# Kernel tuning notes

Measured on AMD Instinct MI355X. Metric: run time of the kernel, lower is better.

Reference implementation:

```python
import jax, jax.numpy as jnp
import numpy as np

N, E, H_DIM, HEADS = 20000, 640000, 128, 8
HD = H_DIM // HEADS  # head_dim = 16


def setup_inputs() -> dict:
    key = jax.random.key(0)
    ks = jax.random.split(key, 12)
    def xavier(k, shape):
        fan_in, fan_out = shape[0], shape[1]
        lim = jnp.sqrt(6.0 / (fan_in + fan_out))
        return jax.random.uniform(k, shape, jnp.float32, -lim, lim)
    return {
        "x": jax.random.normal(ks[0], (N, H_DIM), jnp.float32),
        "edge_index": jax.random.randint(ks[1], (2, E), 0, N, jnp.int64 if jax.config.x64_enabled else jnp.int32),
        "edge_attr": jax.random.normal(ks[2], (E, H_DIM), jnp.float32),
        "WQ": xavier(ks[3], (H_DIM, H_DIM)),
        "WK": xavier(ks[4], (H_DIM, H_DIM)),
        "WV": xavier(ks[5], (H_DIM, H_DIM)),
        "WE": xavier(ks[6], (H_DIM, H_DIM)),
        "Wout": xavier(ks[7], (H_DIM, H_DIM)),
        "bout": jnp.zeros((H_DIM,), jnp.float32),
        "gn_w": jnp.ones((H_DIM,), jnp.float32),
        "gn_b": jnp.zeros((H_DIM,), jnp.float32),
        "gn_ms": jnp.ones((H_DIM,), jnp.float32),
    }


def reference(x, edge_index, edge_attr, WQ, WK, WV, WE, Wout, bout, gn_w, gn_b, gn_ms):
    n = x.shape[0]
    src, dst = edge_index[0], edge_index[1]  # PyG: row=source j, col=target i

    q = (x @ WQ).reshape(n, HEADS, HD)
    k = (x @ WK).reshape(n, HEADS, HD)
    v = (x @ WV).reshape(n, HEADS, HD)
    e = (edge_attr @ WE).reshape(-1, HEADS, HD)

    # per-edge attention score [E, HEADS]
    score = jnp.sum(q[dst] * (k[src] + e), axis=-1) / jnp.sqrt(jnp.asarray(HD, x.dtype))

    # scatter-softmax over edges grouped by destination node
    seg_max = jax.ops.segment_max(score, dst, num_segments=n)  # [N, HEADS]
    seg_max = jnp.where(jnp.isfinite(seg_max), seg_max, 0.0)
    ex = jnp.exp(score - seg_max[dst])
    denom = jax.ops.segment_sum(ex, dst, num_segments=n)
    alpha = ex / (denom[dst] + 1e-16)  # [E, HEADS]

    # weighted scatter-add aggregation
    msg = alpha[..., None] * (v[src] + e)  # [E, HEADS, HD]
    out = jax.ops.segment_sum(msg, dst, num_segments=n).reshape(n, H_DIM)

    out = out @ Wout + bout
    h = out + x  # residual (DropPath is identity in eval)

    # GraphNorm with batch=None -> single-graph normalization
    mean = jnp.mean(h, axis=0)
    o = h - mean * gn_ms
    var = jnp.mean(o * o, axis=0)
    o = gn_w * o / jnp.sqrt(var + 1e-5) + gn_b

    return jax.nn.gelu(o, approximate=False)
```

## Files before the change

kernel.cpp:

```cpp
#include <hip/hip_runtime.h>

using u16 = unsigned short;
using u32 = unsigned int;
typedef float f32x4 __attribute__((ext_vector_type(4)));
typedef float f32x2 __attribute__((ext_vector_type(2)));
typedef short s16x8 __attribute__((ext_vector_type(8)));
typedef u32   u32x2 __attribute__((ext_vector_type(2)));
typedef u32   u32x4 __attribute__((ext_vector_type(4)));

__device__ __forceinline__ u16 f2bf(float f) {
  u32 u = __float_as_uint(f);
  u += 0x7fffu + ((u >> 16) & 1u);
  return (u16)(u >> 16);
}
__device__ __forceinline__ float bf2f(u16 h) {
  return __uint_as_float(((u32)h) << 16);
}

__global__ void ROEN_Final_33526514713351_kernel() {}


__global__ void roen_prep_w(const float* __restrict__ W0, const float* __restrict__ W1,
                            const float* __restrict__ W2, const float* __restrict__ W3,
                            const float* __restrict__ W4, u16* __restrict__ Wt,
                            int* __restrict__ count, int N, float* __restrict__ dbg) {
  int b = blockIdx.x;
  if (b < 5) {
    if (b == 0 && threadIdx.x == 0) dbg[4] = 1004.0f;
    const float* W = (b == 0) ? W0 : (b == 1) ? W1 : (b == 2) ? W2 : (b == 3) ? W3 : W4;
    for (int idx = threadIdx.x; idx < 16384; idx += 256) {
      int n = idx >> 7, k = idx & 127;
      Wt[b * 16384 + idx] = f2bf(W[k * 128 + n]);
    }
  } else {
    int i = (b - 5) * 256 + threadIdx.x;
    if (i == 0) dbg[0] = 1000.0f;
    if (i < N) count[i] = 0;
  }
}

__global__ void roen_hist(const int* __restrict__ ei, int E, int* __restrict__ count,
                          int* __restrict__ rank, float* __restrict__ dbg) {
  int i = blockIdx.x * 256 + threadIdx.x;
  if (i == 0) dbg[1] = 1001.0f;
  if (i < E) rank[i] = atomicAdd(&count[ei[E + i]], 1);
}

__global__ __launch_bounds__(1024) void roen_scan(const int* __restrict__ count, int N,
                                                  int* __restrict__ off,
                                                  float* __restrict__ dbg) {
  __shared__ int wsum[16];
  __shared__ int carrys;
  int tid = threadIdx.x, lane = tid & 63, wv = tid >> 6;
  if (tid == 0) { dbg[2] = 1002.0f; carrys = 0; }
  __syncthreads();
  for (int base = 0; base < N; base += 1024) {
    int i = base + tid;
    int v = (i < N) ? count[i] : 0;
    int x = v;
#pragma unroll
    for (int s = 1; s < 64; s <<= 1) {
      int t = __shfl_up(x, s);
      if (lane >= s) x += t;
    }
    if (lane == 63) wsum[wv] = x;
    __syncthreads();
    if (wv == 0 && lane < 16) {
      int y = wsum[lane];
#pragma unroll
      for (int s = 1; s < 16; s <<= 1) {
        int t = __shfl_up(y, s);
        if (lane >= s) y += t;
      }
      wsum[lane] = y;
    }
    __syncthreads();
    int wbase = (wv == 0) ? 0 : wsum[wv - 1];
    int incl = x + wbase + carrys;
    if (i < N) off[i] = incl - v;
    __syncthreads();
    if (tid == 1023) carrys = incl;
    __syncthreads();
  }
  if (tid == 0) off[N] = carrys;
}

__global__ void roen_scatter(const int* __restrict__ ei, const int* __restrict__ off,
                             const int* __restrict__ rank, int E,
                             int* __restrict__ inv, int* __restrict__ srcS,
                             int* __restrict__ dstS, float* __restrict__ dbg) {
  int i = blockIdx.x * 256 + threadIdx.x;
  if (i == 0) dbg[3] = 1003.0f;
  if (i < E) {
    int d = ei[E + i];
    int p = off[d] + rank[i];
    inv[i] = p;
    srcS[p] = ei[i];
    dstS[p] = d;
  }
}

__global__ __launch_bounds__(256) void roen_gemm_qkv(const float* __restrict__ x,
                                                     const u16* __restrict__ Wt,
                                                     u16* __restrict__ qb, u16* __restrict__ kb,
                                                     u32* __restrict__ vb2, int M,
                                                     float* __restrict__ dbg) {
  __shared__ u16 As[64 * 128];
  const int tid = threadIdx.x;
  if (blockIdx.x == 0 && tid == 0) dbg[5] = 1005.0f;
  const long brow = (long)blockIdx.x * 64;

  {
    f32x4 tmp[8];
#pragma unroll
    for (int j = 0; j < 8; ++j) {
      int idx = j * 256 + tid;
      int row = idx >> 5;
      int c4 = (idx & 31) * 4;
      long grow = brow + row;
      f32x4 a = {0.f, 0.f, 0.f, 0.f};
      if (grow < M) a = *(const f32x4*)(x + grow * 128 + c4);
      tmp[j] = a;
    }
#pragma unroll
    for (int j = 0; j < 8; ++j) {
      int idx = j * 256 + tid;
      int row = idx >> 5;
      int c4 = (idx & 31) * 4;
      u32 lo = ((u32)f2bf(tmp[j][1]) << 16) | (u32)f2bf(tmp[j][0]);
      u32 hi = ((u32)f2bf(tmp[j][3]) << 16) | (u32)f2bf(tmp[j][2]);
      int byte = (row * 256 + c4 * 2) ^ ((row & 7) << 4);
      u32x2 val; val[0] = lo; val[1] = hi;
      *(u32x2*)((char*)As + byte) = val;
    }
  }
  __syncthreads();

  const int wave = tid >> 6, lane = tid & 63;
  const int wc = wave * 32;
  const int lr = lane & 15, lg = lane >> 4;

  s16x8 af[4][4];
#pragma unroll
  for (int ks = 0; ks < 4; ++ks) {
    int kb2 = (ks * 32 + lg * 8) * 2;
#pragma unroll
    for (int mt = 0; mt < 4; ++mt) {
      int row = mt * 16 + lr;
      int byte = (row * 256 + kb2) ^ ((row & 7) << 4);
      af[ks][mt] = *(const s16x8*)((const char*)As + byte);
    }
  }

  for (int w = 0; w < 3; ++w) {
    s16x8 bfr[4][2];
#pragma unroll
    for (int ks = 0; ks < 4; ++ks)
#pragma unroll
      for (int nt = 0; nt < 2; ++nt)
        bfr[ks][nt] = *(const s16x8*)(Wt + w * 16384 + (wc + nt * 16 + lr) * 128 + ks * 32 + lg * 8);

    f32x4 acc[4][2];
    for (int mt = 0; mt < 4; ++mt)
      for (int nt = 0; nt < 2; ++nt) acc[mt][nt] = {0.f, 0.f, 0.f, 0.f};

#pragma unroll
    for (int ks = 0; ks < 4; ++ks)
      for (int mt = 0; mt < 4; ++mt)
        for (int nt = 0; nt < 2; ++nt)
          acc[mt][nt] = __builtin_amdgcn_mfma_f32_16x16x32_bf16(af[ks][mt], bfr[ks][nt], acc[mt][nt], 0, 0, 0);

    if (w == 2) {
      for (int mt = 0; mt < 4; ++mt) {
        for (int r = 0; r < 4; ++r) {
          long row = brow + mt * 16 + lg * 4 + r;
          if (row < M) {
            u32 val = (u32)f2bf(acc[mt][0][r]) | ((u32)f2bf(acc[mt][1][r]) << 16);
            vb2[row * 64 + wave * 16 + lr] = val;
          }
        }
      }
    } else {
      u16* C = (w == 0) ? qb : kb;
      for (int mt = 0; mt < 4; ++mt) {
        for (int nt = 0; nt < 2; ++nt) {
          int col = wc + nt * 16 + lr;
          for (int r = 0; r < 4; ++r) {
            long row = brow + mt * 16 + lg * 4 + r;
            if (row < M) C[row * 128 + col] = f2bf(acc[mt][nt][r]);
          }
        }
      }
    }
  }
}

__global__ __launch_bounds__(256) void roen_gemm_e(const float* __restrict__ ea,
                                                   const u16* __restrict__ WtE,
                                                   const int* __restrict__ inv,
                                                   u32* __restrict__ eS2, int E,
                                                   float* __restrict__ dbg) {
  __shared__ u16 As[64 * 128];
  __shared__ int invv[64];
  const int tid = threadIdx.x;
  if (blockIdx.x == 0 && tid == 0) dbg[6] = 1006.0f;
  const long brow = (long)blockIdx.x * 64;

  if (tid < 64) {
    long pos = brow + tid;
    invv[tid] = (pos < E) ? inv[pos] : -1;
  }

  {
    f32x4 tmp[8];
#pragma unroll
    for (int j = 0; j < 8; ++j) {
      int idx = j * 256 + tid;
      int row = idx >> 5;
      int c4 = (idx & 31) * 4;
      long grow = brow + row;
      f32x4 a = {0.f, 0.f, 0.f, 0.f};
      if (grow < E) a = *(const f32x4*)(ea + grow * 128 + c4);
      tmp[j] = a;
    }
#pragma unroll
    for (int j = 0; j < 8; ++j) {
      int idx = j * 256 + tid;
      int row = idx >> 5;
      int c4 = (idx & 31) * 4;
      u32 lo = ((u32)f2bf(tmp[j][1]) << 16) | (u32)f2bf(tmp[j][0]);
      u32 hi = ((u32)f2bf(tmp[j][3]) << 16) | (u32)f2bf(tmp[j][2]);
      int byte = (row * 256 + c4 * 2) ^ ((row & 7) << 4);
      u32x2 val; val[0] = lo; val[1] = hi;
      *(u32x2*)((char*)As + byte) = val;
    }
  }
  __syncthreads();

  const int wave = tid >> 6, lane = tid & 63;
  const int wc = wave * 32;
  const int lr = lane & 15, lg = lane >> 4;

  s16x8 bfr[4][2];
#pragma unroll
  for (int ks = 0; ks < 4; ++ks)
#pragma unroll
    for (int nt = 0; nt < 2; ++nt)
      bfr[ks][nt] = *(const s16x8*)(WtE + (wc + nt * 16 + lr) * 128 + ks * 32 + lg * 8);

  f32x4 acc[4][2];
  for (int mt = 0; mt < 4; ++mt)
    for (int nt = 0; nt < 2; ++nt) acc[mt][nt] = {0.f, 0.f, 0.f, 0.f};

  for (int ks = 0; ks < 4; ++ks) {
    int kb2 = (ks * 32 + lg * 8) * 2;
    s16x8 af[4];
    for (int mt = 0; mt < 4; ++mt) {
      int row = mt * 16 + lr;
      int byte = (row * 256 + kb2) ^ ((row & 7) << 4);
      af[mt] = *(const s16x8*)((const char*)As + byte);
    }
    for (int mt = 0; mt < 4; ++mt)
      for (int nt = 0; nt < 2; ++nt)
        acc[mt][nt] = __builtin_amdgcn_mfma_f32_16x16x32_bf16(af[mt], bfr[ks][nt], acc[mt][nt], 0, 0, 0);
  }

  for (int mt = 0; mt < 4; ++mt) {
    for (int r = 0; r < 4; ++r) {
      int row = mt * 16 + lg * 4 + r;
      int op = invv[row];
      if (op >= 0) {
        u32 val = (u32)f2bf(acc[mt][0][r]) | ((u32)f2bf(acc[mt][1][r]) << 16);
        eS2[(long)op * 64 + wave * 16 + lr] = val;
      }
    }
  }
}

__global__ __launch_bounds__(256) void roen_score(const int* __restrict__ srcS,
                                                  const int* __restrict__ dstS,
                                                  const u16* __restrict__ qb,
                                                  const u16* __restrict__ kb,
                                                  const u32* __restrict__ eS2,
                                                  float* __restrict__ wS, int E,
                                                  float* __restrict__ dbg) {
  long gid = (long)blockIdx.x * 256 + threadIdx.x;
  if (gid == 0) dbg[9] = 1009.0f;
  long pos = gid >> 3;
  int h = (int)(gid & 7);
  if (pos >= E) return;
  int dst = dstS[pos], src = srcS[pos];
  const s16x8* qp = (const s16x8*)(qb + (long)dst * 128 + h * 16);
  const s16x8* kp = (const s16x8*)(kb + (long)src * 128 + h * 16);
  const u32x4* ep = (const u32x4*)(eS2 + (long)pos * 64 + (h >> 1) * 16);
  const int sh = (h & 1) * 16;
  float acc = 0.f;
#pragma unroll
  for (int c = 0; c < 2; ++c) {
    s16x8 qv = qp[c], kv = kp[c];
    u32x4 ea_ = ep[c * 2], eb_ = ep[c * 2 + 1];
#pragma unroll
    for (int j = 0; j < 4; ++j) {
      float e0 = bf2f((u16)(ea_[j] >> sh));
      float e1 = bf2f((u16)(eb_[j] >> sh));
      acc += bf2f((u16)qv[j]) * (bf2f((u16)kv[j]) + e0);
      acc += bf2f((u16)qv[j + 4]) * (bf2f((u16)kv[j + 4]) + e1);
    }
  }
  wS[pos * 8 + h] = __expf(fminf(acc * 0.25f, 80.f));
}

__global__ __launch_bounds__(256) void roen_node_agg(const int* __restrict__ off,
                                                     const int* __restrict__ srcS,
                                                     const u32* __restrict__ eS2,
                                                     const u32* __restrict__ vb2,
                                                     const float* __restrict__ wS,
                                                     u16* __restrict__ outat, int N,
                                                     float* __restrict__ dbg) {
  int wave = threadIdx.x >> 6;
  int lane = threadIdx.x & 63;
  int node = blockIdx.x * 4 + wave;
  if (node == 0 && lane == 0) dbg[10] = 1010.0f;
  if (node >= N) return;
  int beg = off[node], end = off[node + 1];

  const int dA = 32 * (lane >> 4) + (lane & 15);
  const int dB = dA + 16;
  const int hA = dA >> 4;
  float accA = 0.f, accB = 0.f, dsA = 0.f, dsB = 0.f;

  int pos = beg;
  for (; pos + 8 <= end; pos += 8) {
    int ss[8];
    f32x2 w[8];
    u32 ev[8], vv[8];
#pragma unroll
    for (int i = 0; i < 8; ++i) ss[i] = srcS[pos + i];
#pragma unroll
    for (int i = 0; i < 8; ++i) w[i] = *(const f32x2*)(wS + (long)(pos + i) * 8 + hA);
#pragma unroll
    for (int i = 0; i < 8; ++i) ev[i] = eS2[(long)(pos + i) * 64 + lane];
#pragma unroll
    for (int i = 0; i < 8; ++i) vv[i] = vb2[(long)ss[i] * 64 + lane];
#pragma unroll
    for (int i = 0; i < 8; ++i) {
      accA += w[i][0] * (bf2f((u16)vv[i]) + bf2f((u16)ev[i]));
      accB += w[i][1] * (bf2f((u16)(vv[i] >> 16)) + bf2f((u16)(ev[i] >> 16)));
      dsA += w[i][0]; dsB += w[i][1];
    }
  }
  for (; pos < end; ++pos) {
    f32x2 w = *(const f32x2*)(wS + (long)pos * 8 + hA);
    u32 ev = eS2[(long)pos * 64 + lane];
    int src = srcS[pos];
    u32 vv = vb2[(long)src * 64 + lane];
    accA += w[0] * (bf2f((u16)vv) + bf2f((u16)ev));
    accB += w[1] * (bf2f((u16)(vv >> 16)) + bf2f((u16)(ev >> 16)));
    dsA += w[0]; dsB += w[1];
  }
  outat[(long)node * 128 + dA] = f2bf(accA / (dsA + 1e-16f));
  outat[(long)node * 128 + dB] = f2bf(accB / (dsB + 1e-16f));
}

__global__ __launch_bounds__(256) void roen_gemm_out(const u16* __restrict__ A,
                                                     const u16* __restrict__ Wt,
                                                     const float* __restrict__ x,
                                                     const float* __restrict__ bo,
                                                     float* __restrict__ h,
                                                     float* __restrict__ psum,
                                                     float* __restrict__ psumsq, int M,
                                                     float* __restrict__ dbg) {
  __shared__ u16 As[64 * 128];
  const int tid = threadIdx.x;
  if (blockIdx.x == 0 && tid == 0) dbg[11] = 1011.0f;
  const long brow = (long)blockIdx.x * 64;

#pragma unroll
  for (int j = 0; j < 4; ++j) {
    int idx = j * 256 + tid;
    int row = idx >> 4;
    int c8 = (idx & 15) * 8;
    long grow = brow + row;
    s16x8 val = {0, 0, 0, 0, 0, 0, 0, 0};
    if (grow < M) val = *(const s16x8*)(A + grow * 128 + c8);
    int byte = (row * 256 + c8 * 2) ^ ((row & 7) << 4);
    *(s16x8*)((char*)As + byte) = val;
  }

  const int wave = tid >> 6, lane = tid & 63;
  const int wc = wave * 32;
  const int lr = lane & 15, lg = lane >> 4;

  s16x8 bfr[4][2];
#pragma unroll
  for (int ks = 0; ks < 4; ++ks)
#pragma unroll
    for (int nt = 0; nt < 2; ++nt)
      bfr[ks][nt] = *(const s16x8*)(Wt + (wc + nt * 16 + lr) * 128 + ks * 32 + lg * 8);

  __syncthreads();

  f32x4 acc[4][2];
  for (int mt = 0; mt < 4; ++mt)
    for (int nt = 0; nt < 2; ++nt) acc[mt][nt] = {0.f, 0.f, 0.f, 0.f};

  for (int ks = 0; ks < 4; ++ks) {
    int kb2 = (ks * 32 + lg * 8) * 2;
    s16x8 af[4];
    for (int mt = 0; mt < 4; ++mt) {
      int row = mt * 16 + lr;
      int byte = (row * 256 + kb2) ^ ((row & 7) << 4);
      af[mt] = *(const s16x8*)((const char*)As + byte);
    }
    for (int mt = 0; mt < 4; ++mt)
      for (int nt = 0; nt < 2; ++nt)
        acc[mt][nt] = __builtin_amdgcn_mfma_f32_16x16x32_bf16(af[mt], bfr[ks][nt], acc[mt][nt], 0, 0, 0);
  }

  float b0 = bo[wc + lr];
  float b1 = bo[wc + 16 + lr];
  float cs[2] = {0.f, 0.f}, cs2[2] = {0.f, 0.f};
  for (int mt = 0; mt < 4; ++mt) {
    for (int nt = 0; nt < 2; ++nt) {
      int col = wc + nt * 16 + lr;
      float bb = (nt == 0) ? b0 : b1;
      for (int r = 0; r < 4; ++r) {
        long row = brow + mt * 16 + lg * 4 + r;
        if (row < M) {
          long idx = row * 128 + col;
          float val = acc[mt][nt][r] + bb + x[idx];
          h[idx] = val;
          cs[nt] += val;
          cs2[nt] += val * val;
        }
      }
    }
  }
#pragma unroll
  for (int nt = 0; nt < 2; ++nt) {
    cs[nt] += __shfl_xor(cs[nt], 16);
    cs[nt] += __shfl_xor(cs[nt], 32);
    cs2[nt] += __shfl_xor(cs2[nt], 16);
    cs2[nt] += __shfl_xor(cs2[nt], 32);
  }
  if (lg == 0) {
    int col0 = wc + lr;
    psum[(long)blockIdx.x * 128 + col0] = cs[0];
    psumsq[(long)blockIdx.x * 128 + col0] = cs2[0];
    psum[(long)blockIdx.x * 128 + col0 + 16] = cs[1];
    psumsq[(long)blockIdx.x * 128 + col0 + 16] = cs2[1];
  }
}

__global__ void roen_stats(const float* __restrict__ psum, const float* __restrict__ psumsq,
                           const float* __restrict__ gnw, const float* __restrict__ gnb,
                           const float* __restrict__ gnms, float* __restrict__ Ac,
                           float* __restrict__ Bc, int nb, int N, float* __restrict__ dbg) {
  int d = threadIdx.x;
  if (d == 0) dbg[13] = 1013.0f;
  float s = 0.f, s2 = 0.f;
  for (int i = 0; i < nb; ++i) {
    s += psum[(long)i * 128 + d];
    s2 += psumsq[(long)i * 128 + d];
  }
  float mean = s / (float)N;
  float mm = mean * gnms[d];
  float var = s2 / (float)N - 2.f * mm * mean + mm * mm;
  float scale = gnw[d] * rsqrtf(var + 1e-5f);
  Ac[d] = scale;
  Bc[d] = gnb[d] - mm * scale;
}

__global__ __launch_bounds__(256) void roen_final(const float* __restrict__ h,
                                                  const float* __restrict__ Ac,
                                                  const float* __restrict__ Bc,
                                                  float* __restrict__ out, long total) {
  long i = (long)blockIdx.x * 256 + threadIdx.x;
  if (i >= total) return;
  int d = (int)(i & 127);
  float v = h[i] * Ac[d] + Bc[d];
  out[i] = 0.5f * v * (1.f + erff(v * 0.70710678f));
}

extern "C" void kernel_launch(void* const* d_in, const int* in_sizes, int n_in,
                              void* d_out, int out_size, void* d_ws, size_t ws_size,
                              hipStream_t stream) {
  const float* x   = (const float*)d_in[0];
  const int*   ei  = (const int*)d_in[1];
  const float* ea  = (const float*)d_in[2];
  const float* WQ  = (const float*)d_in[3];
  const float* WK  = (const float*)d_in[4];
  const float* WV  = (const float*)d_in[5];
  const float* WE  = (const float*)d_in[6];
  const float* Wo  = (const float*)d_in[7];
  const float* bo  = (const float*)d_in[8];
  const float* gnw = (const float*)d_in[9];
  const float* gnb = (const float*)d_in[10];
  const float* gnms= (const float*)d_in[11];
  float* out = (float*)d_out;
  float* dbg = (float*)d_out;

  const int N = in_sizes[0] / 128;
  const int E = in_sizes[1] / 2;
  const int gN = (N + 63) / 64;

  char* base = (char*)d_ws;
  size_t cur = 0;
  auto alloc = [&](size_t bytes) -> char* {
    char* r = base + cur;
    cur = (cur + bytes + 255) & ~(size_t)255;
    return r;
  };
  u16*   wt     = (u16*)alloc(5 * 16384 * sizeof(u16));
  u16*   qb     = (u16*)alloc((size_t)N * 128 * sizeof(u16));
  u16*   kb     = (u16*)alloc((size_t)N * 128 * sizeof(u16));
  u32*   vb2    = (u32*)alloc((size_t)N * 64 * sizeof(u32));
  float* wS     = (float*)alloc((size_t)E * 8 * sizeof(float));
  int*   count  = (int*)alloc((size_t)N * sizeof(int));
  int*   offar  = (int*)alloc((size_t)(N + 1) * sizeof(int));
  int*   rank   = (int*)alloc((size_t)E * sizeof(int));
  int*   invar  = (int*)alloc((size_t)E * sizeof(int));
  int*   srcS   = (int*)alloc((size_t)E * sizeof(int));
  int*   dstS   = (int*)alloc((size_t)E * sizeof(int));
  u16*   outat  = (u16*)alloc((size_t)N * 128 * sizeof(u16));
  float* psum   = (float*)alloc((size_t)gN * 128 * sizeof(float));
  float* psumsq = (float*)alloc((size_t)gN * 128 * sizeof(float));
  float* Ac     = (float*)alloc(128 * sizeof(float));
  float* Bc     = (float*)alloc(128 * sizeof(float));
  u32*   eS2    = (u32*)alloc((size_t)E * 64 * sizeof(u32));
  float* hbuf   = (float*)eS2;

  roen_prep_w<<<5 + (N + 255) / 256, 256, 0, stream>>>(WQ, WK, WV, WE, Wo, wt, count, N, dbg);
  roen_hist<<<(E + 255) / 256, 256, 0, stream>>>(ei, E, count, rank, dbg);
  roen_scan<<<1, 1024, 0, stream>>>(count, N, offar, dbg);
  roen_scatter<<<(E + 255) / 256, 256, 0, stream>>>(ei, offar, rank, E, invar, srcS, dstS, dbg);

  roen_gemm_qkv<<<gN, 256, 0, stream>>>(x, wt, qb, kb, vb2, N, dbg);
  roen_gemm_e<<<(E + 63) / 64, 256, 0, stream>>>(ea, wt + 3 * 16384, invar, eS2, E, dbg);

  roen_score<<<(int)(((long)E * 8 + 255) / 256), 256, 0, stream>>>(srcS, dstS, qb, kb, eS2, wS, E, dbg);
  roen_node_agg<<<(N + 3) / 4, 256, 0, stream>>>(offar, srcS, eS2, vb2, wS, outat, N, dbg);

  roen_gemm_out<<<gN, 256, 0, stream>>>(outat, wt + 4 * 16384, x, bo, hbuf, psum, psumsq, N, dbg);
  roen_stats<<<1, 128, 0, stream>>>(psum, psumsq, gnw, gnb, gnms, Ac, Bc, gN, N, dbg);
  roen_final<<<(int)(((long)N * 128 + 255) / 256), 256, 0, stream>>>(hbuf, Ac, Bc, out, (long)N * 128);
}
```

Measured before the change: 414.3 us.

## Keep edge features in original order and gather via sorted permutation in aggregation

Instead of scattering projected edge features into destination-sorted order during the edge GEMM, the GEMM writes rows in original edge order and the scatter kernel emits a sorted-position to edge-id permutation. The score kernel reads edge_index directly, and node aggregation gathers edge features and weights through the permutation. This removes scattered writes and the dstS array, but turns contiguous reads in aggregation into indexed gathers.

```diff
diff --git a/kernel.cpp b/kernel.cpp
--- a/kernel.cpp
+++ b/kernel.cpp
@@ -87,16 +87,15 @@
 
 __global__ void roen_scatter(const int* __restrict__ ei, const int* __restrict__ off,
                              const int* __restrict__ rank, int E,
-                             int* __restrict__ inv, int* __restrict__ srcS,
-                             int* __restrict__ dstS, float* __restrict__ dbg) {
+                             int* __restrict__ sorted, int* __restrict__ srcS,
+                             float* __restrict__ dbg) {
   int i = blockIdx.x * 256 + threadIdx.x;
   if (i == 0) dbg[3] = 1003.0f;
   if (i < E) {
     int d = ei[E + i];
     int p = off[d] + rank[i];
-    inv[i] = p;
+    sorted[p] = i;
     srcS[p] = ei[i];
-    dstS[p] = d;
   }
 }
 
@@ -197,19 +196,12 @@
 
 __global__ __launch_bounds__(256) void roen_gemm_e(const float* __restrict__ ea,
                                                    const u16* __restrict__ WtE,
-                                                   const int* __restrict__ inv,
                                                    u32* __restrict__ eS2, int E,
                                                    float* __restrict__ dbg) {
   __shared__ u16 As[64 * 128];
-  __shared__ int invv[64];
   const int tid = threadIdx.x;
   if (blockIdx.x == 0 && tid == 0) dbg[6] = 1006.0f;
   const long brow = (long)blockIdx.x * 64;
-
-  if (tid < 64) {
-    long pos = brow + tid;
-    invv[tid] = (pos < E) ? inv[pos] : -1;
-  }
 
   {
     f32x4 tmp[8];
@@ -267,18 +259,16 @@
 
   for (int mt = 0; mt < 4; ++mt) {
     for (int r = 0; r < 4; ++r) {
-      int row = mt * 16 + lg * 4 + r;
-      int op = invv[row];
-      if (op >= 0) {
+      long row = brow + mt * 16 + lg * 4 + r;
+      if (row < E) {
         u32 val = (u32)f2bf(acc[mt][0][r]) | ((u32)f2bf(acc[mt][1][r]) << 16);
-        eS2[(long)op * 64 + wave * 16 + lr] = val;
+        eS2[row * 64 + wave * 16 + lr] = val;
       }
     }
   }
 }
 
-__global__ __launch_bounds__(256) void roen_score(const int* __restrict__ srcS,
-                                                  const int* __restrict__ dstS,
+__global__ __launch_bounds__(256) void roen_score(const int* __restrict__ ei,
                                                   const u16* __restrict__ qb,
                                                   const u16* __restrict__ kb,
                                                   const u32* __restrict__ eS2,
@@ -286,13 +276,13 @@
                                                   float* __restrict__ dbg) {
   long gid = (long)blockIdx.x * 256 + threadIdx.x;
   if (gid == 0) dbg[9] = 1009.0f;
-  long pos = gid >> 3;
+  long eid = gid >> 3;
   int h = (int)(gid & 7);
-  if (pos >= E) return;
-  int dst = dstS[pos], src = srcS[pos];
+  if (eid >= E) return;
+  int src = ei[eid], dst = ei[E + eid];
   const s16x8* qp = (const s16x8*)(qb + (long)dst * 128 + h * 16);
   const s16x8* kp = (const s16x8*)(kb + (long)src * 128 + h * 16);
-  const u32x4* ep = (const u32x4*)(eS2 + (long)pos * 64 + (h >> 1) * 16);
+  const u32x4* ep = (const u32x4*)(eS2 + eid * 64 + (h >> 1) * 16);
   const int sh = (h & 1) * 16;
   float acc = 0.f;
 #pragma unroll
@@ -307,10 +297,11 @@
       acc += bf2f((u16)qv[j + 4]) * (bf2f((u16)kv[j + 4]) + e1);
     }
   }
-  wS[pos * 8 + h] = __expf(fminf(acc * 0.25f, 80.f));
+  wS[eid * 8 + h] = __expf(fminf(acc * 0.25f, 80.f));
 }
 
 __global__ __launch_bounds__(256) void roen_node_agg(const int* __restrict__ off,
+                                                     const int* __restrict__ sorted,
                                                      const int* __restrict__ srcS,
                                                      const u32* __restrict__ eS2,
                                                      const u32* __restrict__ vb2,
@@ -331,15 +322,17 @@
 
   int pos = beg;
   for (; pos + 8 <= end; pos += 8) {
-    int ss[8];
+    int eid[8], ss[8];
+#pragma unroll
+    for (int i = 0; i < 8; ++i) eid[i] = sorted[pos + i];
+#pragma unroll
+    for (int i = 0; i < 8; ++i) ss[i] = srcS[pos + i];
     f32x2 w[8];
     u32 ev[8], vv[8];
 #pragma unroll
-    for (int i = 0; i < 8; ++i) ss[i] = srcS[pos + i];
-#pragma unroll
-    for (int i = 0; i < 8; ++i) w[i] = *(const f32x2*)(wS + (long)(pos + i) * 8 + hA);
-#pragma unroll
-    for (int i = 0; i < 8; ++i) ev[i] = eS2[(long)(pos + i) * 64 + lane];
+    for (int i = 0; i < 8; ++i) w[i] = *(const f32x2*)(wS + (long)eid[i] * 8 + hA);
+#pragma unroll
+    for (int i = 0; i < 8; ++i) ev[i] = eS2[(long)eid[i] * 64 + lane];
 #pragma unroll
     for (int i = 0; i < 8; ++i) vv[i] = vb2[(long)ss[i] * 64 + lane];
 #pragma unroll
@@ -350,9 +343,10 @@
     }
   }
   for (; pos < end; ++pos) {
-    f32x2 w = *(const f32x2*)(wS + (long)pos * 8 + hA);
-    u32 ev = eS2[(long)pos * 64 + lane];
+    int eid = sorted[pos];
     int src = srcS[pos];
+    f32x2 w = *(const f32x2*)(wS + (long)eid * 8 + hA);
+    u32 ev = eS2[(long)eid * 64 + lane];
     u32 vv = vb2[(long)src * 64 + lane];
     accA += w[0] * (bf2f((u16)vv) + bf2f((u16)ev));
     accB += w[1] * (bf2f((u16)(vv >> 16)) + bf2f((u16)(ev >> 16)));
@@ -519,9 +513,8 @@
   int*   count  = (int*)alloc((size_t)N * sizeof(int));
   int*   offar  = (int*)alloc((size_t)(N + 1) * sizeof(int));
   int*   rank   = (int*)alloc((size_t)E * sizeof(int));
-  int*   invar  = (int*)alloc((size_t)E * sizeof(int));
+  int*   sorted = (int*)alloc((size_t)E * sizeof(int));
   int*   srcS   = (int*)alloc((size_t)E * sizeof(int));
-  int*   dstS   = (int*)alloc((size_t)E * sizeof(int));
   u16*   outat  = (u16*)alloc((size_t)N * 128 * sizeof(u16));
   float* psum   = (float*)alloc((size_t)gN * 128 * sizeof(float));
   float* psumsq = (float*)alloc((size_t)gN * 128 * sizeof(float));
@@ -533,13 +526,13 @@
   roen_prep_w<<<5 + (N + 255) / 256, 256, 0, stream>>>(WQ, WK, WV, WE, Wo, wt, count, N, dbg);
   roen_hist<<<(E + 255) / 256, 256, 0, stream>>>(ei, E, count, rank, dbg);
   roen_scan<<<1, 1024, 0, stream>>>(count, N, offar, dbg);
-  roen_scatter<<<(E + 255) / 256, 256, 0, stream>>>(ei, offar, rank, E, invar, srcS, dstS, dbg);
+  roen_scatter<<<(E + 255) / 256, 256, 0, stream>>>(ei, offar, rank, E, sorted, srcS, dbg);
 
   roen_gemm_qkv<<<gN, 256, 0, stream>>>(x, wt, qb, kb, vb2, N, dbg);
-  roen_gemm_e<<<(E + 63) / 64, 256, 0, stream>>>(ea, wt + 3 * 16384, invar, eS2, E, dbg);
-
-  roen_score<<<(int)(((long)E * 8 + 255) / 256), 256, 0, stream>>>(srcS, dstS, qb, kb, eS2, wS, E, dbg);
-  roen_node_agg<<<(N + 3) / 4, 256, 0, stream>>>(offar, srcS, eS2, vb2, wS, outat, N, dbg);
+  roen_gemm_e<<<(E + 63) / 64, 256, 0, stream>>>(ea, wt + 3 * 16384, eS2, E, dbg);
+
+  roen_score<<<(int)(((long)E * 8 + 255) / 256), 256, 0, stream>>>(ei, qb, kb, eS2, wS, E, dbg);
+  roen_node_agg<<<(N + 3) / 4, 256, 0, stream>>>(offar, sorted, srcS, eS2, vb2, wS, outat, N, dbg);
 
   roen_gemm_out<<<gN, 256, 0, stream>>>(outat, wt + 4 * 16384, x, bo, hbuf, psum, psumsq, N, dbg);
   roen_stats<<<1, 128, 0, stream>>>(psum, psumsq, gnw, gnb, gnms, Ac, Bc, gN, N, dbg);
```

Measured after the change: 422.1 us. About the same (+1.9%).
